# Optimization experiments

Measured on AMD Instinct MI355X. Metric: run time of the kernel, lower is better.

The kernel has to match this reference:

```python
import jax, jax.numpy as jnp
import numpy as np
import math

BS, NPOS, D_IN = 8, 384, 512
H, D_OUT = 8, 512
DK = D_OUT // H  # 64


def setup_inputs() -> dict:
    key = jax.random.key(0)
    ks = jax.random.split(key, 13)
    s = 0.02
    return {
        "q": jax.random.normal(ks[0], (BS, NPOS, D_IN), jnp.float32),
        "k": jax.random.normal(ks[1], (BS, NPOS, D_IN), jnp.float32),
        "v": jax.random.normal(ks[2], (BS, NPOS, D_IN), jnp.float32),
        "rpos_k": jax.random.normal(ks[3], (NPOS, NPOS, H, DK), jnp.float32) * s,
        "rpos_v": jax.random.normal(ks[4], (NPOS, NPOS, H, DK), jnp.float32) * s,
        "Wq": jax.random.normal(ks[5], (D_IN, D_OUT), jnp.float32) * s,
        "bq": jnp.zeros((D_OUT,), jnp.float32),
        "Wk": jax.random.normal(ks[6], (D_IN, D_OUT), jnp.float32) * s,
        "bk": jnp.zeros((D_OUT,), jnp.float32),
        "Wv": jax.random.normal(ks[7], (D_IN, D_OUT), jnp.float32) * s,
        "bv": jnp.zeros((D_OUT,), jnp.float32),
        "Wo": jax.random.normal(ks[8], (D_OUT, D_OUT), jnp.float32) * s,
        "bo": jnp.zeros((D_OUT,), jnp.float32),
    }


def reference(q, k, v, rpos_k, rpos_v, Wq, bq, Wk, bk, Wv, bv, Wo, bo):
    # model_name = 'with_pe' path; mask=None; dropout in eval mode (no-op)
    bs = q.shape[0]
    inv_sqrt_dk = 1.0 / math.sqrt(DK)

    qh = (q @ Wq + bq).reshape(bs, -1, H, DK).transpose(0, 2, 1, 3)  # bs,h,n,dk
    kh = (k @ Wk + bk).reshape(bs, -1, H, DK).transpose(0, 2, 1, 3)
    original_v = v @ Wv + bv                                          # bs,n,d_out
    vh = original_v.reshape(bs, -1, H, DK).transpose(0, 2, 1, 3)

    # standard content-content scores
    std_scores = jnp.einsum('bhnd,bhmd->bhnm', qh, kh) * inv_sqrt_dk
    # relative-position scores: q_n . rpos_k[n, m, h] -- computed inline,
    # no bs-broadcast materialization of rpos_k
    pos_scores = jnp.einsum('bhnd,nmhd->bhnm', qh, rpos_k) * inv_sqrt_dk

    scores = jax.nn.softmax(std_scores + pos_scores, axis=-1)
    # NOTE: original code divides the attention output by sqrt(d_k) again
    attn_out = jnp.einsum('bhnm,bhmd->bhnd', scores, vh) * inv_sqrt_dk

    concat = attn_out.transpose(0, 2, 1, 3).reshape(bs, -1, D_OUT)
    output = concat @ Wo + bo
    return (original_v, output)
```

## Files before the change

### kernel.cpp

```cpp
#include <hip/hip_runtime.h>

#define NPOS 384
#define DMODEL 512
#define NH 8
#define DK 64
#define BS 8
#define MROWS (BS * NPOS)
#define SROW (NPOS * NPOS)

typedef __attribute__((ext_vector_type(8))) short bf16x8;
typedef __attribute__((ext_vector_type(4))) float f32x4;

__device__ __forceinline__ unsigned short f2bf(float x) {
  unsigned int u = __float_as_uint(x);
  return (unsigned short)((u + 0x7fffu + ((u >> 16) & 1u)) >> 16);
}
__device__ __forceinline__ unsigned int pk2(float lo, float hi) {
  unsigned int ul = __float_as_uint(lo), uh = __float_as_uint(hi);
  ul = (ul + 0x7fffu + ((ul >> 16) & 1u)) >> 16;
  uh = (uh + 0x7fffu + ((uh >> 16) & 1u)) & 0xffff0000u;
  return ul | uh;
}
__device__ __forceinline__ bf16x8 pack8(float4 a, float4 b) {
  union { uint4 u; bf16x8 v; } cv;
  cv.u = make_uint4(pk2(a.x, a.y), pk2(a.z, a.w), pk2(b.x, b.y), pk2(b.z, b.w));
  return cv.v;
}

__global__ __launch_bounds__(256) void convert_w(
    const float* __restrict__ Wq, const float* __restrict__ Wk,
    const float* __restrict__ Wv, const float* __restrict__ Wo,
    unsigned short* __restrict__ wt) {
  __shared__ float s[64][68];
  const int z = blockIdx.z;
  const float* W = z == 0 ? Wq : z == 1 ? Wk : z == 2 ? Wv : Wo;
  unsigned short* out = wt + (size_t)z * DMODEL * DMODEL;
  const int k0 = blockIdx.x * 64, n0 = blockIdx.y * 64;
  const int t = threadIdx.x;
#pragma unroll
  for (int i = 0; i < 4; ++i) {
    int f = t + i * 256;
    int kr = f >> 4, q4 = f & 15;
    *(float4*)&s[kr][q4 * 4] = *(const float4*)&W[(size_t)(k0 + kr) * DMODEL + n0 + q4 * 4];
  }
  __syncthreads();
#pragma unroll
  for (int i = 0; i < 2; ++i) {
    int slot = t + i * 256;
    int n = slot >> 3, kq = slot & 7;
    unsigned int p[4];
#pragma unroll
    for (int j = 0; j < 4; ++j)
      p[j] = pk2(s[kq * 8 + j * 2][n], s[kq * 8 + j * 2 + 1][n]);
    *(uint4*)&out[(size_t)(n0 + n) * DMODEL + k0 + kq * 8] = make_uint4(p[0], p[1], p[2], p[3]);
  }
}

__global__ __launch_bounds__(256) void convert_in(
    const float* __restrict__ qin, const float* __restrict__ kin,
    const float* __restrict__ vin, unsigned short* __restrict__ qkvb) {
  const int z = blockIdx.y;
  const float* src = z == 0 ? qin : z == 1 ? kin : vin;
  unsigned short* dst = qkvb + (size_t)z * MROWS * DMODEL;
  const size_t i = ((size_t)blockIdx.x * 256 + threadIdx.x) * 8;
  float4 a = *(const float4*)&src[i];
  float4 b = *(const float4*)&src[i + 4];
  union { uint4 u; bf16x8 v; } cv;
  cv.u = make_uint4(pk2(a.x, a.y), pk2(a.z, a.w), pk2(b.x, b.y), pk2(b.z, b.w));
  *(uint4*)&dst[i] = cv.u;
}

__global__ __launch_bounds__(256) void proj_qkv(
    const unsigned short* __restrict__ qkvb,
    const unsigned short* __restrict__ wt,
    const float* __restrict__ bq, const float* __restrict__ bk, const float* __restrict__ bv,
    unsigned short* __restrict__ qhb, unsigned short* __restrict__ khb,
    float* __restrict__ origv, unsigned short* __restrict__ vhT) {
  __shared__ unsigned short As[64][72];
  __shared__ unsigned short Bs[64][72];
  const int z = blockIdx.z;
  const unsigned short* A = qkvb + (size_t)z * MROWS * DMODEL;
  const unsigned short* Wt = wt + (size_t)z * DMODEL * DMODEL;
  const float* bias = z == 0 ? bq : z == 1 ? bk : bv;
  const int m0 = blockIdx.x * 64, n0 = blockIdx.y * 64;
  const int t = threadIdx.x, lane = t & 63, w = t >> 6;
  const int wr = w >> 1, wc = w & 1;
  const int l15 = lane & 15, l4 = lane >> 4;
  f32x4 acc[2][2] = {};
  for (int kt = 0; kt < 8; ++kt) {
    const int k0 = kt * 64;
#pragma unroll
    for (int i = 0; i < 2; ++i) {
      int s = t + i * 256;
      int row = s >> 3, kq = s & 7;
      *(uint4*)&As[row][kq * 8] = *(const uint4*)&A[(size_t)(m0 + row) * DMODEL + k0 + kq * 8];
      *(uint4*)&Bs[row][kq * 8] = *(const uint4*)&Wt[(size_t)(n0 + row) * DMODEL + k0 + kq * 8];
    }
    __syncthreads();
    bf16x8 af[2][2], bfr[2][2];
#pragma unroll
    for (int mf = 0; mf < 2; ++mf)
#pragma unroll
      for (int ks = 0; ks < 2; ++ks)
        af[mf][ks] = *(const bf16x8*)&As[wr * 32 + mf * 16 + l15][ks * 32 + l4 * 8];
#pragma unroll
    for (int nf = 0; nf < 2; ++nf)
#pragma unroll
      for (int ks = 0; ks < 2; ++ks)
        bfr[nf][ks] = *(const bf16x8*)&Bs[wc * 32 + nf * 16 + l15][ks * 32 + l4 * 8];
#pragma unroll
    for (int mf = 0; mf < 2; ++mf)
#pragma unroll
      for (int nf = 0; nf < 2; ++nf)
#pragma unroll
        for (int ks = 0; ks < 2; ++ks)
          acc[mf][nf] = __builtin_amdgcn_mfma_f32_16x16x32_bf16(af[mf][ks], bfr[nf][ks],
                                                                acc[mf][nf], 0, 0, 0);
    __syncthreads();
  }
#pragma unroll
  for (int mf = 0; mf < 2; ++mf)
#pragma unroll
    for (int nf = 0; nf < 2; ++nf) {
      const int row0 = m0 + wr * 32 + mf * 16 + l4 * 4;
      const int col = n0 + wc * 32 + nf * 16 + l15;
      const float bi = bias[col];
      if (z == 0) {
#pragma unroll
        for (int i = 0; i < 4; ++i)
          qhb[(size_t)(row0 + i) * DMODEL + col] = f2bf((acc[mf][nf][i] + bi) * 0.125f);
      } else if (z == 1) {
#pragma unroll
        for (int i = 0; i < 4; ++i)
          khb[(size_t)(row0 + i) * DMODEL + col] = f2bf(acc[mf][nf][i] + bi);
      } else {
        const int b = row0 / NPOS, n = row0 - b * NPOS;
        const int h = col >> 6, d = col & 63;
        float vals[4];
#pragma unroll
        for (int i = 0; i < 4; ++i) {
          vals[i] = acc[mf][nf][i] + bi;
          origv[(size_t)(row0 + i) * DMODEL + col] = vals[i];
        }
        ushort4 pk;
        pk.x = f2bf(vals[0]); pk.y = f2bf(vals[1]);
        pk.z = f2bf(vals[2]); pk.w = f2bf(vals[3]);
        *(ushort4*)&vhT[((size_t)((b * NH + h) * DK + d)) * NPOS + n] = pk;
      }
    }
}

__global__ __launch_bounds__(256) void scores_nt(
    const unsigned short* __restrict__ qhb, const unsigned short* __restrict__ khb,
    float* __restrict__ scores) {
  __shared__ unsigned short As[128][72];
  __shared__ unsigned short Bs[128][72];
  const int z = blockIdx.z, b = z >> 3, h = z & 7;
  const unsigned short* Ag = qhb + (size_t)b * NPOS * DMODEL + h * DK;
  const unsigned short* Bg = khb + (size_t)b * NPOS * DMODEL + h * DK;
  const int n0 = blockIdx.x * 128, m0 = blockIdx.y * 128;
  const int t = threadIdx.x, lane = t & 63, w = t >> 6;
  const int wr = w >> 1, wc = w & 1;
  const int l15 = lane & 15, l4 = lane >> 4;
#pragma unroll
  for (int i = 0; i < 4; ++i) {
    int s = t + i * 256;
    int row = s >> 3, kq = s & 7;
    *(uint4*)&As[row][kq * 8] = *(const uint4*)&Ag[(size_t)(n0 + row) * DMODEL + kq * 8];
    *(uint4*)&Bs[row][kq * 8] = *(const uint4*)&Bg[(size_t)(m0 + row) * DMODEL + kq * 8];
  }
  __syncthreads();
  f32x4 acc[4][4] = {};
  bf16x8 af[4][2], bfr[4][2];
#pragma unroll
  for (int mf = 0; mf < 4; ++mf)
#pragma unroll
    for (int ks = 0; ks < 2; ++ks)
      af[mf][ks] = *(const bf16x8*)&As[wr * 64 + mf * 16 + l15][ks * 32 + l4 * 8];
#pragma unroll
  for (int nf = 0; nf < 4; ++nf)
#pragma unroll
    for (int ks = 0; ks < 2; ++ks)
      bfr[nf][ks] = *(const bf16x8*)&Bs[wc * 64 + nf * 16 + l15][ks * 32 + l4 * 8];
#pragma unroll
  for (int mf = 0; mf < 4; ++mf)
#pragma unroll
    for (int nf = 0; nf < 4; ++nf)
#pragma unroll
      for (int ks = 0; ks < 2; ++ks)
        acc[mf][nf] = __builtin_amdgcn_mfma_f32_16x16x32_bf16(af[mf][ks], bfr[nf][ks],
                                                              acc[mf][nf], 0, 0, 0);
  float* C = scores + (size_t)z * SROW;
#pragma unroll
  for (int mf = 0; mf < 4; ++mf)
#pragma unroll
    for (int nf = 0; nf < 4; ++nf) {
      int rown = n0 + wr * 64 + mf * 16 + l4 * 4;
      int colm = m0 + wc * 64 + nf * 16 + l15;
#pragma unroll
      for (int i = 0; i < 4; ++i)
        C[(size_t)(rown + i) * NPOS + colm] = acc[mf][nf][i];
    }
}

__global__ __launch_bounds__(256) void pos_scores_mfma(
    const unsigned short* __restrict__ qhb,
    const float* __restrict__ rk,
    float* __restrict__ scores) {
  const int n = blockIdx.y;
  const int m0 = blockIdx.x * 16;
  const int t = threadIdx.x, lane = t & 63, w = t >> 6;
  const int l15 = lane & 15, l4 = lane >> 4;
  const int bcol = l15 & 7;
  const float* rkrow = rk + ((size_t)n * NPOS + m0 + l15) * (NH * DK);
  const unsigned short* qp = qhb + ((size_t)bcol * NPOS + n) * DMODEL;
#pragma unroll
  for (int hp = 0; hp < 2; ++hp) {
    const int h = w * 2 + hp;
    const int base = h * DK;
    f32x4 acc = {};
#pragma unroll
    for (int ks = 0; ks < 2; ++ks) {
      const int off = base + ks * 32 + l4 * 8;
      const float4 ra = *(const float4*)&rkrow[off];
      const float4 rb = *(const float4*)&rkrow[off + 4];
      bf16x8 af = pack8(ra, rb);
      bf16x8 bfr = *(const bf16x8*)&qp[off];
      acc = __builtin_amdgcn_mfma_f32_16x16x32_bf16(af, bfr, acc, 0, 0, 0);
    }
    if (l15 < 8) {
      float* srow = scores + ((size_t)(l15 * NH + h) * NPOS + n) * NPOS + m0 + l4 * 4;
      float4 c = *(float4*)srow;
      c.x += acc[0]; c.y += acc[1]; c.z += acc[2]; c.w += acc[3];
      *(float4*)srow = c;
    }
  }
}

__global__ __launch_bounds__(256) void softmax_bf(float* __restrict__ scores) {
  const int row = blockIdx.x * 4 + (threadIdx.x >> 6);
  const int lane = threadIdx.x & 63;
  float* s = scores + (size_t)row * NPOS;
  unsigned short* p = (unsigned short*)s;
  float v[6];
  float mx = -1e30f;
#pragma unroll
  for (int j = 0; j < 6; ++j) {
    v[j] = s[j * 64 + lane];
    mx = fmaxf(mx, v[j]);
  }
#pragma unroll
  for (int o = 32; o; o >>= 1) mx = fmaxf(mx, __shfl_xor(mx, o, 64));
  float sum = 0.f;
#pragma unroll
  for (int j = 0; j < 6; ++j) {
    v[j] = __expf(v[j] - mx);
    sum += v[j];
  }
#pragma unroll
  for (int o = 32; o; o >>= 1) sum += __shfl_xor(sum, o, 64);
  const float inv = 0.125f / sum;
#pragma unroll
  for (int j = 0; j < 6; ++j) p[j * 64 + lane] = f2bf(v[j] * inv);
}

__global__ __launch_bounds__(256) void pv_nt(
    const unsigned short* __restrict__ Pbase,
    const unsigned short* __restrict__ vhT,
    unsigned short* __restrict__ attb) {
  __shared__ unsigned short As[64][72];
  __shared__ unsigned short Bs[64][72];
  const int z = blockIdx.z, b = z >> 3, h = z & 7;
  const int n0 = blockIdx.x * 64;
  const unsigned short* Ag = Pbase + ((size_t)(z * NPOS + n0)) * 768;
  const unsigned short* Bg = vhT + (size_t)z * DK * NPOS;
  const int t = threadIdx.x, lane = t & 63, w = t >> 6;
  const int wr = w >> 1, wc = w & 1;
  const int l15 = lane & 15, l4 = lane >> 4;
  f32x4 acc[2][2] = {};
  for (int kt = 0; kt < 6; ++kt) {
    const int k0 = kt * 64;
#pragma unroll
    for (int i = 0; i < 2; ++i) {
      int s = t + i * 256;
      int row = s >> 3, kq = s & 7;
      *(uint4*)&As[row][kq * 8] = *(const uint4*)&Ag[(size_t)row * 768 + k0 + kq * 8];
      *(uint4*)&Bs[row][kq * 8] = *(const uint4*)&Bg[(size_t)row * NPOS + k0 + kq * 8];
    }
    __syncthreads();
    bf16x8 af[2][2], bfr[2][2];
#pragma unroll
    for (int mf = 0; mf < 2; ++mf)
#pragma unroll
      for (int ks = 0; ks < 2; ++ks)
        af[mf][ks] = *(const bf16x8*)&As[wr * 32 + mf * 16 + l15][ks * 32 + l4 * 8];
#pragma unroll
    for (int nf = 0; nf < 2; ++nf)
#pragma unroll
      for (int ks = 0; ks < 2; ++ks)
        bfr[nf][ks] = *(const bf16x8*)&Bs[wc * 32 + nf * 16 + l15][ks * 32 + l4 * 8];
#pragma unroll
    for (int mf = 0; mf < 2; ++mf)
#pragma unroll
      for (int nf = 0; nf < 2; ++nf)
#pragma unroll
        for (int ks = 0; ks < 2; ++ks)
          acc[mf][nf] = __builtin_amdgcn_mfma_f32_16x16x32_bf16(af[mf][ks], bfr[nf][ks],
                                                                acc[mf][nf], 0, 0, 0);
    __syncthreads();
  }
#pragma unroll
  for (int mf = 0; mf < 2; ++mf)
#pragma unroll
    for (int nf = 0; nf < 2; ++nf) {
      const int n = n0 + wr * 32 + mf * 16 + l4 * 4;
      const int d = wc * 32 + nf * 16 + l15;
#pragma unroll
      for (int i = 0; i < 4; ++i)
        attb[(size_t)(b * NPOS + n + i) * DMODEL + h * DK + d] = f2bf(acc[mf][nf][i]);
    }
}

__global__ __launch_bounds__(256) void proj_o(
    const unsigned short* __restrict__ attb, const unsigned short* __restrict__ WtO,
    const float* __restrict__ bo, float* __restrict__ outp) {
  __shared__ unsigned short As[64][72];
  __shared__ unsigned short Bs[64][72];
  const int m0 = blockIdx.x * 64, n0 = blockIdx.y * 64;
  const int t = threadIdx.x, lane = t & 63, w = t >> 6;
  const int wr = w >> 1, wc = w & 1;
  const int l15 = lane & 15, l4 = lane >> 4;
  f32x4 acc[2][2] = {};
  for (int kt = 0; kt < 8; ++kt) {
    const int k0 = kt * 64;
#pragma unroll
    for (int i = 0; i < 2; ++i) {
      int s = t + i * 256;
      int row = s >> 3, kq = s & 7;
      *(uint4*)&As[row][kq * 8] = *(const uint4*)&attb[(size_t)(m0 + row) * DMODEL + k0 + kq * 8];
      *(uint4*)&Bs[row][kq * 8] = *(const uint4*)&WtO[(size_t)(n0 + row) * DMODEL + k0 + kq * 8];
    }
    __syncthreads();
    bf16x8 af[2][2], bfr[2][2];
#pragma unroll
    for (int mf = 0; mf < 2; ++mf)
#pragma unroll
      for (int ks = 0; ks < 2; ++ks)
        af[mf][ks] = *(const bf16x8*)&As[wr * 32 + mf * 16 + l15][ks * 32 + l4 * 8];
#pragma unroll
    for (int nf = 0; nf < 2; ++nf)
#pragma unroll
      for (int ks = 0; ks < 2; ++ks)
        bfr[nf][ks] = *(const bf16x8*)&Bs[wc * 32 + nf * 16 + l15][ks * 32 + l4 * 8];
#pragma unroll
    for (int mf = 0; mf < 2; ++mf)
#pragma unroll
      for (int nf = 0; nf < 2; ++nf)
#pragma unroll
        for (int ks = 0; ks < 2; ++ks)
          acc[mf][nf] = __builtin_amdgcn_mfma_f32_16x16x32_bf16(af[mf][ks], bfr[nf][ks],
                                                                acc[mf][nf], 0, 0, 0);
    __syncthreads();
  }
#pragma unroll
  for (int mf = 0; mf < 2; ++mf)
#pragma unroll
    for (int nf = 0; nf < 2; ++nf) {
      const int row0 = m0 + wr * 32 + mf * 16 + l4 * 4;
      const int col = n0 + wc * 32 + nf * 16 + l15;
      const float bi = bo[col];
#pragma unroll
      for (int i = 0; i < 4; ++i)
        outp[(size_t)(row0 + i) * DMODEL + col] = acc[mf][nf][i] + bi;
    }
}

extern "C" void kernel_launch(void* const* d_in, const int* in_sizes, int n_in,
                              void* d_out, int out_size, void* d_ws, size_t ws_size,
                              hipStream_t stream) {
  const float* q  = (const float*)d_in[0];
  const float* k  = (const float*)d_in[1];
  const float* v  = (const float*)d_in[2];
  const float* rk = (const float*)d_in[3];
  const float* Wq = (const float*)d_in[5];
  const float* bq = (const float*)d_in[6];
  const float* Wk = (const float*)d_in[7];
  const float* bk = (const float*)d_in[8];
  const float* Wv = (const float*)d_in[9];
  const float* bv = (const float*)d_in[10];
  const float* Wo = (const float*)d_in[11];
  const float* bo = (const float*)d_in[12];

  const size_t TOK = (size_t)MROWS * DMODEL;
  unsigned short* wt   = (unsigned short*)d_ws;
  unsigned short* qhb  = wt + 4 * DMODEL * DMODEL;
  unsigned short* khb  = qhb + TOK;
  unsigned short* vhT  = khb + TOK;
  unsigned short* attb = vhT + TOK;
  float* scores = (float*)(attb + TOK);
  unsigned short* qkvb = (unsigned short*)scores;
  float* origv = (float*)d_out;
  float* outp = origv + TOK;

  dim3 blk(256);

  convert_w<<<dim3(8, 8, 4), blk, 0, stream>>>(Wq, Wk, Wv, Wo, wt);
  convert_in<<<dim3(768, 3), blk, 0, stream>>>(q, k, v, qkvb);
  proj_qkv<<<dim3(48, 8, 3), blk, 0, stream>>>(qkvb, wt, bq, bk, bv,
                                               qhb, khb, origv, vhT);
  scores_nt<<<dim3(3, 3, 64), blk, 0, stream>>>(qhb, khb, scores);
  pos_scores_mfma<<<dim3(24, 384), blk, 0, stream>>>(qhb, rk, scores);
  softmax_bf<<<dim3((BS * NH * NPOS) / 4), blk, 0, stream>>>(scores);
  pv_nt<<<dim3(6, 1, 64), blk, 0, stream>>>((const unsigned short*)scores, vhT, attb);
  proj_o<<<dim3(48, 8), blk, 0, stream>>>(attb, wt + 3 * DMODEL * DMODEL, bo, outp);
}
```

Before: 154.9 us.

## Fuse positional scores into softmax and merge input/weight conversion kernels

The positional-score MFMA kernel is restructured so each block handles one (head, query row) pair across all 384 keys. It stages the positional scores for the 8 batches in shared memory, then runs softmax directly on the content scores plus that tile. This removes the separate read-modify-write of the full fp32 score tensor and a kernel launch. The weight and input bf16 conversion kernels are also merged into one launch, at the cost of idle blocks in the weight branch. The grid shrinks to 8x384 blocks, each doing more serial work.

```diff
diff --git a/kernel.cpp b/kernel.cpp
--- a/kernel.cpp
+++ b/kernel.cpp
@@ -27,16 +27,31 @@
   return cv.v;
 }
 
-__global__ __launch_bounds__(256) void convert_w(
+__global__ __launch_bounds__(256) void convert_all(
+    const float* __restrict__ qin, const float* __restrict__ kin,
+    const float* __restrict__ vin,
     const float* __restrict__ Wq, const float* __restrict__ Wk,
     const float* __restrict__ Wv, const float* __restrict__ Wo,
-    unsigned short* __restrict__ wt) {
+    unsigned short* __restrict__ qkvb, unsigned short* __restrict__ wt) {
+  const int z = blockIdx.y;
+  const int t = threadIdx.x;
+  if (z < 3) {
+    const float* src = z == 0 ? qin : z == 1 ? kin : vin;
+    unsigned short* dst = qkvb + (size_t)z * MROWS * DMODEL;
+    const size_t i = ((size_t)blockIdx.x * 256 + t) * 8;
+    float4 a = *(const float4*)&src[i];
+    float4 b = *(const float4*)&src[i + 4];
+    union { uint4 u; bf16x8 v; } cv;
+    cv.u = make_uint4(pk2(a.x, a.y), pk2(a.z, a.w), pk2(b.x, b.y), pk2(b.z, b.w));
+    *(uint4*)&dst[i] = cv.u;
+    return;
+  }
+  if (blockIdx.x >= 64) return;
   __shared__ float s[64][68];
-  const int z = blockIdx.z;
-  const float* W = z == 0 ? Wq : z == 1 ? Wk : z == 2 ? Wv : Wo;
-  unsigned short* out = wt + (size_t)z * DMODEL * DMODEL;
-  const int k0 = blockIdx.x * 64, n0 = blockIdx.y * 64;
-  const int t = threadIdx.x;
+  const int w = z - 3;
+  const float* W = w == 0 ? Wq : w == 1 ? Wk : w == 2 ? Wv : Wo;
+  unsigned short* out = wt + (size_t)w * DMODEL * DMODEL;
+  const int k0 = (blockIdx.x & 7) * 64, n0 = (blockIdx.x >> 3) * 64;
 #pragma unroll
   for (int i = 0; i < 4; ++i) {
     int f = t + i * 256;
@@ -54,20 +69,6 @@
       p[j] = pk2(s[kq * 8 + j * 2][n], s[kq * 8 + j * 2 + 1][n]);
     *(uint4*)&out[(size_t)(n0 + n) * DMODEL + k0 + kq * 8] = make_uint4(p[0], p[1], p[2], p[3]);
   }
-}
-
-__global__ __launch_bounds__(256) void convert_in(
-    const float* __restrict__ qin, const float* __restrict__ kin,
-    const float* __restrict__ vin, unsigned short* __restrict__ qkvb) {
-  const int z = blockIdx.y;
-  const float* src = z == 0 ? qin : z == 1 ? kin : vin;
-  unsigned short* dst = qkvb + (size_t)z * MROWS * DMODEL;
-  const size_t i = ((size_t)blockIdx.x * 256 + threadIdx.x) * 8;
-  float4 a = *(const float4*)&src[i];
-  float4 b = *(const float4*)&src[i + 4];
-  union { uint4 u; bf16x8 v; } cv;
-  cv.u = make_uint4(pk2(a.x, a.y), pk2(a.z, a.w), pk2(b.x, b.y), pk2(b.z, b.w));
-  *(uint4*)&dst[i] = cv.u;
 }
 
 __global__ __launch_bounds__(256) void proj_qkv(
@@ -203,65 +204,62 @@
     }
 }
 
-__global__ __launch_bounds__(256) void pos_scores_mfma(
+__global__ __launch_bounds__(256) void pos_sm(
     const unsigned short* __restrict__ qhb,
     const float* __restrict__ rk,
     float* __restrict__ scores) {
+  __shared__ float Pf[8][392];
+  const int h = blockIdx.x;
   const int n = blockIdx.y;
-  const int m0 = blockIdx.x * 16;
   const int t = threadIdx.x, lane = t & 63, w = t >> 6;
   const int l15 = lane & 15, l4 = lane >> 4;
   const int bcol = l15 & 7;
-  const float* rkrow = rk + ((size_t)n * NPOS + m0 + l15) * (NH * DK);
-  const unsigned short* qp = qhb + ((size_t)bcol * NPOS + n) * DMODEL;
-#pragma unroll
-  for (int hp = 0; hp < 2; ++hp) {
-    const int h = w * 2 + hp;
-    const int base = h * DK;
+  const unsigned short* qp = qhb + ((size_t)bcol * NPOS + n) * DMODEL + h * DK;
+  const bf16x8 bfr0 = *(const bf16x8*)&qp[l4 * 8];
+  const bf16x8 bfr1 = *(const bf16x8*)&qp[32 + l4 * 8];
+#pragma unroll
+  for (int mt = 0; mt < 6; ++mt) {
+    const int m0 = w * 96 + mt * 16;
+    const float* rkrow = rk + ((size_t)n * NPOS + m0 + l15) * (NH * DK) + h * DK;
     f32x4 acc = {};
-#pragma unroll
-    for (int ks = 0; ks < 2; ++ks) {
-      const int off = base + ks * 32 + l4 * 8;
-      const float4 ra = *(const float4*)&rkrow[off];
-      const float4 rb = *(const float4*)&rkrow[off + 4];
-      bf16x8 af = pack8(ra, rb);
-      bf16x8 bfr = *(const bf16x8*)&qp[off];
-      acc = __builtin_amdgcn_mfma_f32_16x16x32_bf16(af, bfr, acc, 0, 0, 0);
-    }
+    const float4 ra = *(const float4*)&rkrow[l4 * 8];
+    const float4 rb = *(const float4*)&rkrow[l4 * 8 + 4];
+    acc = __builtin_amdgcn_mfma_f32_16x16x32_bf16(pack8(ra, rb), bfr0, acc, 0, 0, 0);
+    const float4 rc = *(const float4*)&rkrow[32 + l4 * 8];
+    const float4 rd = *(const float4*)&rkrow[32 + l4 * 8 + 4];
+    acc = __builtin_amdgcn_mfma_f32_16x16x32_bf16(pack8(rc, rd), bfr1, acc, 0, 0, 0);
     if (l15 < 8) {
-      float* srow = scores + ((size_t)(l15 * NH + h) * NPOS + n) * NPOS + m0 + l4 * 4;
-      float4 c = *(float4*)srow;
-      c.x += acc[0]; c.y += acc[1]; c.z += acc[2]; c.w += acc[3];
-      *(float4*)srow = c;
-    }
-  }
-}
-
-__global__ __launch_bounds__(256) void softmax_bf(float* __restrict__ scores) {
-  const int row = blockIdx.x * 4 + (threadIdx.x >> 6);
-  const int lane = threadIdx.x & 63;
-  float* s = scores + (size_t)row * NPOS;
-  unsigned short* p = (unsigned short*)s;
-  float v[6];
-  float mx = -1e30f;
-#pragma unroll
-  for (int j = 0; j < 6; ++j) {
-    v[j] = s[j * 64 + lane];
-    mx = fmaxf(mx, v[j]);
-  }
-#pragma unroll
-  for (int o = 32; o; o >>= 1) mx = fmaxf(mx, __shfl_xor(mx, o, 64));
-  float sum = 0.f;
-#pragma unroll
-  for (int j = 0; j < 6; ++j) {
-    v[j] = __expf(v[j] - mx);
-    sum += v[j];
-  }
-#pragma unroll
-  for (int o = 32; o; o >>= 1) sum += __shfl_xor(sum, o, 64);
-  const float inv = 0.125f / sum;
-#pragma unroll
-  for (int j = 0; j < 6; ++j) p[j * 64 + lane] = f2bf(v[j] * inv);
+#pragma unroll
+      for (int i = 0; i < 4; ++i) Pf[l15][m0 + l4 * 4 + i] = acc[i];
+    }
+  }
+  __syncthreads();
+#pragma unroll
+  for (int rr = 0; rr < 2; ++rr) {
+    const int b = w * 2 + rr;
+    float* srow = scores + ((size_t)(b * NH + h) * NPOS + n) * NPOS;
+    unsigned short* prow = (unsigned short*)srow;
+    float v[6];
+    float mx = -1e30f;
+#pragma unroll
+    for (int j = 0; j < 6; ++j) {
+      v[j] = srow[j * 64 + lane] + Pf[b][j * 64 + lane];
+      mx = fmaxf(mx, v[j]);
+    }
+#pragma unroll
+    for (int o = 32; o; o >>= 1) mx = fmaxf(mx, __shfl_xor(mx, o, 64));
+    float sum = 0.f;
+#pragma unroll
+    for (int j = 0; j < 6; ++j) {
+      v[j] = __expf(v[j] - mx);
+      sum += v[j];
+    }
+#pragma unroll
+    for (int o = 32; o; o >>= 1) sum += __shfl_xor(sum, o, 64);
+    const float inv = 0.125f / sum;
+#pragma unroll
+    for (int j = 0; j < 6; ++j) prow[j * 64 + lane] = f2bf(v[j] * inv);
+  }
 }
 
 __global__ __launch_bounds__(256) void pv_nt(
@@ -404,13 +402,11 @@
 
   dim3 blk(256);
 
-  convert_w<<<dim3(8, 8, 4), blk, 0, stream>>>(Wq, Wk, Wv, Wo, wt);
-  convert_in<<<dim3(768, 3), blk, 0, stream>>>(q, k, v, qkvb);
+  convert_all<<<dim3(768, 7), blk, 0, stream>>>(q, k, v, Wq, Wk, Wv, Wo, qkvb, wt);
   proj_qkv<<<dim3(48, 8, 3), blk, 0, stream>>>(qkvb, wt, bq, bk, bv,
                                                qhb, khb, origv, vhT);
   scores_nt<<<dim3(3, 3, 64), blk, 0, stream>>>(qhb, khb, scores);
-  pos_scores_mfma<<<dim3(24, 384), blk, 0, stream>>>(qhb, rk, scores);
-  softmax_bf<<<dim3((BS * NH * NPOS) / 4), blk, 0, stream>>>(scores);
+  pos_sm<<<dim3(8, 384), blk, 0, stream>>>(qhb, rk, scores);
   pv_nt<<<dim3(6, 1, 64), blk, 0, stream>>>((const unsigned short*)scores, vhT, attb);
   proj_o<<<dim3(48, 8), blk, 0, stream>>>(attb, wt + 3 * DMODEL * DMODEL, bo, outp);
 }
```

New measurement: 134.4 us. 13.2% less time.
